# Kernel optimization log

Hardware: AMD Instinct MI355X
Metric: run time of the kernel (lower is better)

Reference implementation:

```python
import jax, jax.numpy as jnp
import numpy as np

LEN_HIS = 20   # q_len_his: sliding-window history length
DIM_C = 4      # dim_c
H = 64         # GRU hidden = final_mlp_hidden_width
D = 36         # global_graph_width(32) + goal(2) + action(2)
N = 32768      # total timesteps across many episodes


def setup_inputs() -> dict:
    key = jax.random.key(0)
    ks = jax.random.split(key, 8)
    emb = jax.random.normal(ks[0], (N, D), jnp.float32)
    dones = (jax.random.uniform(ks[1], (N, 1)) < 0.02).astype(jnp.int32)
    s = lambda k, shape, fan: jax.random.normal(k, shape, jnp.float32) / np.sqrt(fan).astype(np.float32)
    return {
        "embeddings": emb,
        "W_ih": s(ks[2], (3 * H, D), D),
        "W_hh": s(ks[3], (3 * H, H), H),
        "b_ih": jnp.zeros((3 * H,), jnp.float32),
        "b_hh": jnp.zeros((3 * H,), jnp.float32),
        "W1": s(ks[4], (H, H), H),
        "b1": jnp.zeros((H,), jnp.float32),
        "W2": s(ks[5], (DIM_C, H), H),
        "b2": jnp.zeros((DIM_C,), jnp.float32),
        "dones": dones,
    }


def _his_calculate_c(embeddings, W_ih, W_hh, b_ih, b_hh, W1, b1, W2, b2, dones):
    """Batched/padded version of the ragged sliding-window GRU+MLP loop.

    For each timestep t, the torch code runs the GRU over
    embeddings[max(episode_start, t-L+1) : t+1] from a zero hidden state,
    then applies FinalPredMLP to the final hidden state.
    """
    n = embeddings.shape[0]
    done = dones[:, 0] != 0
    idx = jnp.arange(n)
    # episode_start[t] = (index of most recent done strictly before t) + 1, else 0
    prev_done = jnp.concatenate([jnp.zeros((1,), bool), done[:-1]])
    ep_start = jax.lax.cummax(jnp.where(prev_done, idx, 0))
    win_start = jnp.maximum(ep_start, idx - LEN_HIS + 1)            # [N]

    # padded windows: position l holds embeddings[t - (L-1) + l]
    gidx = idx[:, None] - (LEN_HIS - 1) + jnp.arange(LEN_HIS)[None, :]  # [N, L]
    valid = gidx >= win_start[:, None]                                   # [N, L]
    X = embeddings[jnp.clip(gidx, 0, n - 1)] * valid[..., None]          # [N, L, D]

    def cell(h, inp):
        x, v = inp                      # x: [N, D], v: [N]
        gi = x @ W_ih.T + b_ih          # [N, 3H]
        gh = h @ W_hh.T + b_hh          # [N, 3H]
        ir, iz, inn = jnp.split(gi, 3, axis=-1)
        hr, hz, hnn = jnp.split(gh, 3, axis=-1)
        r = jax.nn.sigmoid(ir + hr)
        z = jax.nn.sigmoid(iz + hz)
        ncand = jnp.tanh(inn + r * hnn)
        h_new = (1.0 - z) * ncand + z * h
        return jnp.where(v[:, None], h_new, h), None

    h0 = jnp.zeros((n, H), embeddings.dtype)
    hT, _ = jax.lax.scan(cell, h0, (jnp.swapaxes(X, 0, 1), valid.T))  # [N, H]

    # FinalPredMLP: Linear(H,H) -> ReLU -> Linear(H, dim_c)
    hid = jax.nn.relu(hT @ W1.T + b1)
    return hid @ W2.T + b2              # [N, dim_c]


def reference(embeddings, W_ih, W_hh, b_ih, b_hh, W1, b1, W2, b2, dones):
    return _his_calculate_c(embeddings, W_ih, W_hh, b_ih, b_hh, W1, b1, W2, b2, dones)
```

## Files before the change

### kernel.cpp

```cpp
#include <hip/hip_runtime.h>

#define NT 32768
#define DI 36
#define HH 64
#define G3 192
#define LH 20
#define SGS 196

#define NLOG2E -1.4426950408889634f
#define TLOG2E 2.8853900817779268f

#define UNION_OFF  27440
#define SFIRST_OFF 39728
#define SMEM_BYTES 39792

typedef __attribute__((ext_vector_type(8))) short bf16x8;
typedef __attribute__((ext_vector_type(4))) float f32x4;
typedef __attribute__((ext_vector_type(4))) int int4v;
union frag_cast { int4v i4; bf16x8 h8; };

__device__ __forceinline__ unsigned f2u(float f) { union { float f; unsigned u; } x; x.f = f; return x.u; }
__device__ __forceinline__ float u2f(unsigned u) { union { float f; unsigned u; } x; x.u = u; return x.f; }
__device__ __forceinline__ unsigned short f2bf_rne(float f) {
    union { float f; unsigned u; } x; x.f = f;
    unsigned r = x.u + 0x7FFFu + ((x.u >> 16) & 1u);
    return (unsigned short)(r >> 16);
}

__global__ __launch_bounds__(64) void prep_kernel(
    const float* __restrict__ W_ih, const float* __restrict__ W_hh,
    const float* __restrict__ W1, int4v* __restrict__ wfrag)
{
    const int b = (int)blockIdx.x;
    const int l = (int)threadIdx.x;
    unsigned short e[8];
    if (b < 72) {
        const int set = b / 24, fb = b % 24;
        const int mt = fb >> 1, kt = fb & 1;
        const int m = mt * 16 + (l & 15);
        const float sc = ((mt >> 2) < 2) ? NLOG2E : TLOG2E;
        const int k0 = kt * 32 + (l >> 4) * 8;
#pragma unroll
        for (int jj = 0; jj < 8; ++jj) {
            const int k = k0 + jj;
            if (set == 2) {
                e[jj] = f2bf_rne(W_hh[(size_t)m * HH + k] * sc);
            } else {
                const float v = (k < DI) ? W_ih[(size_t)m * DI + k] * sc : 0.f;
                const unsigned u = f2u(v);
                if (set == 0) e[jj] = (unsigned short)(u >> 16);
                else          e[jj] = (unsigned short)(f2u(v - u2f(u & 0xFFFF0000u)) >> 16);
            }
        }
    } else {
        const int bb = b - 72;
        const bool is_lo = bb >= 8;
        const int f = bb & 7;
        const int mt = f >> 1, kt = f & 1;
        const int m = mt * 16 + (l & 15);
        const int k0 = kt * 32 + (l >> 4) * 8;
#pragma unroll
        for (int jj = 0; jj < 8; ++jj) {
            const float v = W1[(size_t)m * HH + k0 + jj];
            const unsigned u = f2u(v);
            if (!is_lo) e[jj] = (unsigned short)(u >> 16);
            else        e[jj] = (unsigned short)(f2u(v - u2f(u & 0xFFFF0000u)) >> 16);
        }
    }
    int4v p;
    p.x = e[0] | ((unsigned)e[1] << 16); p.y = e[2] | ((unsigned)e[3] << 16);
    p.z = e[4] | ((unsigned)e[5] << 16); p.w = e[6] | ((unsigned)e[7] << 16);
    wfrag[b * 64 + l] = p;
}

__global__ __launch_bounds__(256, 4) void gru_kernel(
    const float* __restrict__ emb, const int4v* __restrict__ wfrag,
    const float* __restrict__ b_ih, const float* __restrict__ b_hh,
    const float* __restrict__ b1, const float* __restrict__ W2,
    const float* __restrict__ b2, const int* __restrict__ dones,
    float* __restrict__ out)
{
    __shared__ __align__(16) char SMEM[SMEM_BYTES];
    float* const Sg = (float*)SMEM;
    unsigned short* const EmbH = (unsigned short*)(SMEM + UNION_OFF);
    unsigned short* const EmbL = EmbH + 48 * 64;
    unsigned short* const HbB  = (unsigned short*)(SMEM + UNION_OFF);
    unsigned short* const HfH  = (unsigned short*)(SMEM + UNION_OFF);
    unsigned short* const HfL  = HfH + 1152;
    int* const sfirst = (int*)(SMEM + SFIRST_OFF);

    const int tid = threadIdx.x;
    const int lane = tid & 63;
    const int W = tid >> 6;
    const int li = lane & 15;
    const int q = lane >> 4;
    const int blk = ((int)blockIdx.x & 7) * 256 + ((int)blockIdx.x >> 3);
    const int T0 = blk * 16;

    {
        int4v* z = (int4v*)EmbH;
        for (int i = tid; i < 768; i += 256) z[i] = int4v{0, 0, 0, 0};
    }
    if (tid < 16) {
        const int tt = T0 + tid;
        int lo = tt - (LH - 1); if (lo < 0) lo = 0;
        int ws = lo;
        for (int j = lo; j < tt; ++j)
            ws = (dones[j] != 0) ? (j + 1) : ws;
        sfirst[tid] = ws - (tt - (LH - 1));
    }
    __syncthreads();
    for (int i = tid; i < 35 * DI; i += 256) {
        const int r = i / DI, c = i % DI;
        int tt = T0 - (LH - 1) + r; tt = tt < 0 ? 0 : tt;
        const float v = emb[(size_t)tt * DI + c];
        const unsigned u = f2u(v);
        EmbH[r * 64 + c] = (unsigned short)(u >> 16);
        EmbL[r * 64 + c] = (unsigned short)(f2u(v - u2f(u & 0xFFFF0000u)) >> 16);
    }

    bf16x8 aih[3][2], ail[3][2], whh[3][2];
#pragma unroll
    for (int g = 0; g < 3; ++g)
#pragma unroll
        for (int kt = 0; kt < 2; ++kt) {
            const int fb = (4 * g + W) * 2 + kt;
            frag_cast a, b, c;
            a.i4 = wfrag[(0 * 24 + fb) * 64 + lane];
            b.i4 = wfrag[(1 * 24 + fb) * 64 + lane];
            c.i4 = wfrag[(2 * 24 + fb) * 64 + lane];
            aih[g][kt] = a.h8; ail[g][kt] = b.h8; whh[g][kt] = c.h8;
        }

    const int joff = 16 * W + 4 * q;
    f32x4 biasI[3];
#pragma unroll
    for (int g = 0; g < 3; ++g) {
        const float sc = (g < 2) ? NLOG2E : TLOG2E;
        const f32x4 bi = *(const f32x4*)&b_ih[64 * g + joff];
        if (g < 2) {
            const f32x4 bh = *(const f32x4*)&b_hh[64 * g + joff];
#pragma unroll
            for (int rr = 0; rr < 4; ++rr) biasI[g][rr] = (bi[rr] + bh[rr]) * sc;
        } else {
#pragma unroll
            for (int rr = 0; rr < 4; ++rr) biasI[g][rr] = bi[rr] * sc;
        }
    }
    f32x4 bnv;
    {
        const f32x4 b = *(const f32x4*)&b_hh[128 + joff];
#pragma unroll
        for (int rr = 0; rr < 4; ++rr) bnv[rr] = b[rr] * TLOG2E;
    }
    __syncthreads();

#pragma unroll
    for (int nt = 0; nt < 3; ++nt) {
        bf16x8 ebh[2], ebl[2];
#pragma unroll
        for (int kt = 0; kt < 2; ++kt) {
            const int idx = (16 * nt + li) * 64 + 32 * kt + 8 * q;
            ebh[kt] = *(const bf16x8*)&EmbH[idx];
            ebl[kt] = *(const bf16x8*)&EmbL[idx];
        }
#pragma unroll
        for (int g = 0; g < 3; ++g) {
            f32x4 a = biasI[g];
            a = __builtin_amdgcn_mfma_f32_16x16x32_bf16(aih[g][0], ebh[0], a, 0, 0, 0);
            a = __builtin_amdgcn_mfma_f32_16x16x32_bf16(aih[g][1], ebh[1], a, 0, 0, 0);
            a = __builtin_amdgcn_mfma_f32_16x16x32_bf16(ail[g][0], ebh[0], a, 0, 0, 0);
            a = __builtin_amdgcn_mfma_f32_16x16x32_bf16(ail[g][1], ebh[1], a, 0, 0, 0);
            a = __builtin_amdgcn_mfma_f32_16x16x32_bf16(aih[g][0], ebl[0], a, 0, 0, 0);
            a = __builtin_amdgcn_mfma_f32_16x16x32_bf16(aih[g][1], ebl[1], a, 0, 0, 0);
            const int row = 16 * nt + li;
            if (row < 35)
                *(f32x4*)&Sg[row * SGS + 64 * g + joff] = a;
        }
    }
    __syncthreads();
    const int sfr = sfirst[li];

    float h[4] = {0.f, 0.f, 0.f, 0.f};
    f32x4 accR, accZ, accN, ginv;
    f32x4 gvR, gvZ, gvN;

    {
        const float* gp = Sg + li * SGS;
        accR = *(const f32x4*)(gp + joff);
        accZ = *(const f32x4*)(gp + 64 + joff);
        ginv = *(const f32x4*)(gp + 128 + joff);
        accN = bnv;
        const bool valid = (0 >= sfr);
#pragma unroll
        for (int rr = 0; rr < 4; ++rr) {
            const float r  = __builtin_amdgcn_rcpf(1.f + __builtin_amdgcn_exp2f(accR[rr]));
            const float z  = __builtin_amdgcn_rcpf(1.f + __builtin_amdgcn_exp2f(accZ[rr]));
            const float nc = 1.f - 2.f * __builtin_amdgcn_rcpf(1.f + __builtin_amdgcn_exp2f(ginv[rr] + r * accN[rr]));
            h[rr] = valid ? fmaf(z, 0.f - nc, nc) : 0.f;
        }
        uint2 ph;
        ph.x = __builtin_amdgcn_perm(f2u(h[1]), f2u(h[0]), 0x07060302u);
        ph.y = __builtin_amdgcn_perm(f2u(h[3]), f2u(h[2]), 0x07060302u);
        *(uint2*)&HbB[1152 + li * 72 + joff] = ph;
        const float* gq = Sg + (li + 1) * SGS;
        gvR = *(const f32x4*)(gq + joff);
        gvZ = *(const f32x4*)(gq + 64 + joff);
        gvN = *(const f32x4*)(gq + 128 + joff);
    }
    __syncthreads();

#pragma unroll 2
    for (int s = 1; s < LH; ++s) {
        const int rb = s & 1;
        const bf16x8 bh0 = *(const bf16x8*)&HbB[rb * 1152 + li * 72 + 8 * q];
        const bf16x8 bh1 = *(const bf16x8*)&HbB[rb * 1152 + li * 72 + 32 + 8 * q];

        accR = gvR; accZ = gvZ; ginv = gvN; accN = bnv;
        {
            int r = li + s + 1; r = r > 34 ? 34 : r;
            const float* gq = Sg + r * SGS;
            gvR = *(const f32x4*)(gq + joff);
            gvZ = *(const f32x4*)(gq + 64 + joff);
            gvN = *(const f32x4*)(gq + 128 + joff);
        }
#pragma unroll
        for (int g = 0; g < 3; ++g) {
            f32x4 a = (g == 0) ? accR : (g == 1) ? accZ : accN;
            a = __builtin_amdgcn_mfma_f32_16x16x32_bf16(whh[g][0], bh0, a, 0, 0, 0);
            a = __builtin_amdgcn_mfma_f32_16x16x32_bf16(whh[g][1], bh1, a, 0, 0, 0);
            if (g == 0) accR = a; else if (g == 1) accZ = a; else accN = a;
        }
        const bool valid = (s >= sfr);
#pragma unroll
        for (int rr = 0; rr < 4; ++rr) {
            const float r  = __builtin_amdgcn_rcpf(1.f + __builtin_amdgcn_exp2f(accR[rr]));
            const float z  = __builtin_amdgcn_rcpf(1.f + __builtin_amdgcn_exp2f(accZ[rr]));
            const float nc = 1.f - 2.f * __builtin_amdgcn_rcpf(1.f + __builtin_amdgcn_exp2f(ginv[rr] + r * accN[rr]));
            const float hn = fmaf(z, h[rr] - nc, nc);
            h[rr] = valid ? hn : h[rr];
        }
        if (s != LH - 1) {
            uint2 ph;
            ph.x = __builtin_amdgcn_perm(f2u(h[1]), f2u(h[0]), 0x07060302u);
            ph.y = __builtin_amdgcn_perm(f2u(h[3]), f2u(h[2]), 0x07060302u);
            *(uint2*)&HbB[(1 - rb) * 1152 + li * 72 + joff] = ph;
        }
        __syncthreads();
    }

    {
        const unsigned u0 = f2u(h[0]), u1 = f2u(h[1]);
        const unsigned u2 = f2u(h[2]), u3 = f2u(h[3]);
        uint2 ph, pl;
        ph.x = __builtin_amdgcn_perm(u1, u0, 0x07060302u);
        ph.y = __builtin_amdgcn_perm(u3, u2, 0x07060302u);
        const unsigned l0 = f2u(h[0] - u2f(u0 & 0xFFFF0000u));
        const unsigned l1 = f2u(h[1] - u2f(u1 & 0xFFFF0000u));
        const unsigned l2 = f2u(h[2] - u2f(u2 & 0xFFFF0000u));
        const unsigned l3 = f2u(h[3] - u2f(u3 & 0xFFFF0000u));
        pl.x = __builtin_amdgcn_perm(l1, l0, 0x07060302u);
        pl.y = __builtin_amdgcn_perm(l3, l2, 0x07060302u);
        *(uint2*)&HfH[li * 72 + joff] = ph;
        *(uint2*)&HfL[li * 72 + joff] = pl;
    }
    __syncthreads();
    {
        bf16x8 w1h[2], w1l[2];
#pragma unroll
        for (int kt = 0; kt < 2; ++kt) {
            frag_cast a, b;
            a.i4 = wfrag[(72 + W * 2 + kt) * 64 + lane];
            b.i4 = wfrag[(80 + W * 2 + kt) * 64 + lane];
            w1h[kt] = a.h8; w1l[kt] = b.h8;
        }
        const bf16x8 bh0 = *(const bf16x8*)&HfH[li * 72 + 8 * q];
        const bf16x8 bh1 = *(const bf16x8*)&HfH[li * 72 + 32 + 8 * q];
        const bf16x8 bl0 = *(const bf16x8*)&HfL[li * 72 + 8 * q];
        const bf16x8 bl1 = *(const bf16x8*)&HfL[li * 72 + 32 + 8 * q];
        f32x4 a = *(const f32x4*)&b1[joff];
        a = __builtin_amdgcn_mfma_f32_16x16x32_bf16(w1h[0], bh0, a, 0, 0, 0);
        a = __builtin_amdgcn_mfma_f32_16x16x32_bf16(w1h[1], bh1, a, 0, 0, 0);
        a = __builtin_amdgcn_mfma_f32_16x16x32_bf16(w1l[0], bh0, a, 0, 0, 0);
        a = __builtin_amdgcn_mfma_f32_16x16x32_bf16(w1l[1], bh1, a, 0, 0, 0);
        a = __builtin_amdgcn_mfma_f32_16x16x32_bf16(w1h[0], bl0, a, 0, 0, 0);
        a = __builtin_amdgcn_mfma_f32_16x16x32_bf16(w1h[1], bl1, a, 0, 0, 0);
        __syncthreads();
        float4 st;
        st.x = fmaxf(a[0], 0.f); st.y = fmaxf(a[1], 0.f);
        st.z = fmaxf(a[2], 0.f); st.w = fmaxf(a[3], 0.f);
        *(float4*)&Sg[li * 68 + joff] = st;
    }
    __syncthreads();
    if (tid < 64) {
        const int tt = tid >> 2, c = tid & 3;
        float o2 = b2[c];
        for (int m4 = 0; m4 < 16; ++m4) {
            const float4 hv = *(const float4*)&Sg[tt * 68 + 4 * m4];
            const float4 wv = *(const float4*)&W2[c * HH + 4 * m4];
            o2 += hv.x * wv.x + hv.y * wv.y + hv.z * wv.z + hv.w * wv.w;
        }
        out[(size_t)(T0 + tt) * 4 + c] = o2;
    }
}

extern "C" void kernel_launch(void* const* d_in, const int* in_sizes, int n_in,
                              void* d_out, int out_size, void* d_ws, size_t ws_size,
                              hipStream_t stream) {
    const float* emb  = (const float*)d_in[0];
    const float* W_ih = (const float*)d_in[1];
    const float* W_hh = (const float*)d_in[2];
    const float* b_ih = (const float*)d_in[3];
    const float* b_hh = (const float*)d_in[4];
    const float* W1   = (const float*)d_in[5];
    const float* b1   = (const float*)d_in[6];
    const float* W2   = (const float*)d_in[7];
    const float* b2   = (const float*)d_in[8];
    const int*   dn   = (const int*)d_in[9];

    int4v* wfrag = (int4v*)d_ws;
    float* o = (float*)d_out;

    prep_kernel<<<88, 64, 0, stream>>>(W_ih, W_hh, W1, wfrag);
    gru_kernel<<<NT / 16, 256, 0, stream>>>(emb, wfrag, b_ih, b_hh,
                                            b1, W2, b2, dn, o);
}
```

Baseline: 114.8 us.

## Shrink LDS embedding staging to one buffer and raise occupancy to five blocks

The separate hi/lo bf16 embedding buffers in shared memory are replaced by one padded buffer (row stride 72). The input projection now runs in two passes: the hi part first, then the lo part is written into the same buffer and accumulated onto the stored gate sums. Global embedding loads are issued into registers before the first barrier, and the W_hh fragments and n-gate bias load are deferred until after the input projection. LDS use drops and launch bounds ask for five blocks per CU, to raise occupancy and hide latency, at the cost of extra barriers, an extra LDS round trip of gate sums, and tighter register limits.

```diff
diff --git a/kernel.cpp b/kernel.cpp
--- a/kernel.cpp
+++ b/kernel.cpp
@@ -11,8 +11,8 @@
 #define TLOG2E 2.8853900817779268f
 
 #define UNION_OFF  27440
-#define SFIRST_OFF 39728
-#define SMEM_BYTES 39792
+#define SFIRST_OFF 32480
+#define SMEM_BYTES 32544
 
 typedef __attribute__((ext_vector_type(8))) short bf16x8;
 typedef __attribute__((ext_vector_type(4))) float f32x4;
@@ -73,7 +73,7 @@
     wfrag[b * 64 + l] = p;
 }
 
-__global__ __launch_bounds__(256, 4) void gru_kernel(
+__global__ __launch_bounds__(256, 5) void gru_kernel(
     const float* __restrict__ emb, const int4v* __restrict__ wfrag,
     const float* __restrict__ b_ih, const float* __restrict__ b_hh,
     const float* __restrict__ b1, const float* __restrict__ W2,
@@ -82,8 +82,7 @@
 {
     __shared__ __align__(16) char SMEM[SMEM_BYTES];
     float* const Sg = (float*)SMEM;
-    unsigned short* const EmbH = (unsigned short*)(SMEM + UNION_OFF);
-    unsigned short* const EmbL = EmbH + 48 * 64;
+    unsigned short* const EmbP = (unsigned short*)(SMEM + UNION_OFF);
     unsigned short* const HbB  = (unsigned short*)(SMEM + UNION_OFF);
     unsigned short* const HfH  = (unsigned short*)(SMEM + UNION_OFF);
     unsigned short* const HfL  = HfH + 1152;
@@ -97,9 +96,19 @@
     const int blk = ((int)blockIdx.x & 7) * 256 + ((int)blockIdx.x >> 3);
     const int T0 = blk * 16;
 
-    {
-        int4v* z = (int4v*)EmbH;
-        for (int i = tid; i < 768; i += 256) z[i] = int4v{0, 0, 0, 0};
+    float ev[5];
+#pragma unroll
+    for (int k = 0; k < 5; ++k) {
+        const int i = tid + 256 * k;
+        if (i < 35 * DI) {
+            const int r = i / DI, c = i % DI;
+            int tt = T0 - (LH - 1) + r; tt = tt < 0 ? 0 : tt;
+            ev[k] = emb[(size_t)tt * DI + c];
+        }
+    }
+    {
+        int4v* z = (int4v*)EmbP;
+        for (int i = tid; i < 315; i += 256) z[i] = int4v{0, 0, 0, 0};
     }
     if (tid < 16) {
         const int tt = T0 + tid;
@@ -110,26 +119,23 @@
         sfirst[tid] = ws - (tt - (LH - 1));
     }
     __syncthreads();
-    for (int i = tid; i < 35 * DI; i += 256) {
-        const int r = i / DI, c = i % DI;
-        int tt = T0 - (LH - 1) + r; tt = tt < 0 ? 0 : tt;
-        const float v = emb[(size_t)tt * DI + c];
-        const unsigned u = f2u(v);
-        EmbH[r * 64 + c] = (unsigned short)(u >> 16);
-        EmbL[r * 64 + c] = (unsigned short)(f2u(v - u2f(u & 0xFFFF0000u)) >> 16);
-    }
-
-    bf16x8 aih[3][2], ail[3][2], whh[3][2];
+#pragma unroll
+    for (int k = 0; k < 5; ++k) {
+        const int i = tid + 256 * k;
+        if (i < 35 * DI)
+            EmbP[(i / DI) * 72 + (i % DI)] = (unsigned short)(f2u(ev[k]) >> 16);
+    }
+
+    bf16x8 aih[3][2], ail[3][2];
 #pragma unroll
     for (int g = 0; g < 3; ++g)
 #pragma unroll
         for (int kt = 0; kt < 2; ++kt) {
             const int fb = (4 * g + W) * 2 + kt;
-            frag_cast a, b, c;
+            frag_cast a, b;
             a.i4 = wfrag[(0 * 24 + fb) * 64 + lane];
             b.i4 = wfrag[(1 * 24 + fb) * 64 + lane];
-            c.i4 = wfrag[(2 * 24 + fb) * 64 + lane];
-            aih[g][kt] = a.h8; ail[g][kt] = b.h8; whh[g][kt] = c.h8;
+            aih[g][kt] = a.h8; ail[g][kt] = b.h8;
         }
 
     const int joff = 16 * W + 4 * q;
@@ -147,23 +153,16 @@
             for (int rr = 0; rr < 4; ++rr) biasI[g][rr] = bi[rr] * sc;
         }
     }
-    f32x4 bnv;
-    {
-        const f32x4 b = *(const f32x4*)&b_hh[128 + joff];
-#pragma unroll
-        for (int rr = 0; rr < 4; ++rr) bnv[rr] = b[rr] * TLOG2E;
-    }
     __syncthreads();
 
 #pragma unroll
     for (int nt = 0; nt < 3; ++nt) {
-        bf16x8 ebh[2], ebl[2];
-#pragma unroll
-        for (int kt = 0; kt < 2; ++kt) {
-            const int idx = (16 * nt + li) * 64 + 32 * kt + 8 * q;
-            ebh[kt] = *(const bf16x8*)&EmbH[idx];
-            ebl[kt] = *(const bf16x8*)&EmbL[idx];
-        }
+        const int row = 16 * nt + li;
+        const int rowr = row < 35 ? row : 34;
+        bf16x8 ebh[2];
+#pragma unroll
+        for (int kt = 0; kt < 2; ++kt)
+            ebh[kt] = *(const bf16x8*)&EmbP[rowr * 72 + 32 * kt + 8 * q];
 #pragma unroll
         for (int g = 0; g < 3; ++g) {
             f32x4 a = biasI[g];
@@ -171,15 +170,56 @@
             a = __builtin_amdgcn_mfma_f32_16x16x32_bf16(aih[g][1], ebh[1], a, 0, 0, 0);
             a = __builtin_amdgcn_mfma_f32_16x16x32_bf16(ail[g][0], ebh[0], a, 0, 0, 0);
             a = __builtin_amdgcn_mfma_f32_16x16x32_bf16(ail[g][1], ebh[1], a, 0, 0, 0);
+            if (row < 35)
+                *(f32x4*)&Sg[row * SGS + 64 * g + joff] = a;
+        }
+    }
+    __syncthreads();
+#pragma unroll
+    for (int k = 0; k < 5; ++k) {
+        const int i = tid + 256 * k;
+        if (i < 35 * DI) {
+            const unsigned u = f2u(ev[k]);
+            EmbP[(i / DI) * 72 + (i % DI)] =
+                (unsigned short)(f2u(ev[k] - u2f(u & 0xFFFF0000u)) >> 16);
+        }
+    }
+    __syncthreads();
+
+#pragma unroll
+    for (int nt = 0; nt < 3; ++nt) {
+        const int row = 16 * nt + li;
+        const int rowr = row < 35 ? row : 34;
+        bf16x8 ebl[2];
+#pragma unroll
+        for (int kt = 0; kt < 2; ++kt)
+            ebl[kt] = *(const bf16x8*)&EmbP[rowr * 72 + 32 * kt + 8 * q];
+#pragma unroll
+        for (int g = 0; g < 3; ++g) {
+            f32x4 a = *(const f32x4*)&Sg[rowr * SGS + 64 * g + joff];
             a = __builtin_amdgcn_mfma_f32_16x16x32_bf16(aih[g][0], ebl[0], a, 0, 0, 0);
             a = __builtin_amdgcn_mfma_f32_16x16x32_bf16(aih[g][1], ebl[1], a, 0, 0, 0);
-            const int row = 16 * nt + li;
             if (row < 35)
                 *(f32x4*)&Sg[row * SGS + 64 * g + joff] = a;
         }
     }
     __syncthreads();
     const int sfr = sfirst[li];
+
+    bf16x8 whh[3][2];
+#pragma unroll
+    for (int g = 0; g < 3; ++g)
+#pragma unroll
+        for (int kt = 0; kt < 2; ++kt) {
+            frag_cast c; c.i4 = wfrag[(48 + (4 * g + W) * 2 + kt) * 64 + lane];
+            whh[g][kt] = c.h8;
+        }
+    f32x4 bnv;
+    {
+        const f32x4 b = *(const f32x4*)&b_hh[128 + joff];
+#pragma unroll
+        for (int rr = 0; rr < 4; ++rr) bnv[rr] = b[rr] * TLOG2E;
+    }
 
     float h[4] = {0.f, 0.f, 0.f, 0.f};
     f32x4 accR, accZ, accN, ginv;
```

New measurement: 116.9 us. About the same (+1.9%).
